# Optimization experiments

Measured on AMD Instinct MI355X. Metric: run time of the kernel, lower is better.

## Reference

```python
import jax, jax.numpy as jnp
import numpy as np

B, Q, K, H = 4, 512, 512, 256

def setup_inputs() -> dict:
    key = jax.random.key(0)
    ks = jax.random.split(key, 6)
    scale = 1.0 / np.sqrt(H)
    return {
        "queries": jax.random.normal(ks[0], (B, Q, H), dtype=jnp.float32),
        "keys": jax.random.normal(ks[1], (B, K, H), dtype=jnp.float32),
        "values": jax.random.normal(ks[2], (B, K, H), dtype=jnp.float32),
        "W_q": jax.random.normal(ks[3], (H, H), dtype=jnp.float32) * scale,
        "W_k": jax.random.normal(ks[4], (H, H), dtype=jnp.float32) * scale,
        "w_v": jax.random.normal(ks[5], (H,), dtype=jnp.float32) * scale,
    }

def reference(queries, keys, values, W_q, W_k, w_v):
    # Linear (no bias): x @ W.T, matching torch nn.Linear convention
    q = jnp.einsum('bqh,oh->bqo', queries, W_q)      # [B,Q,H]
    k = jnp.einsum('bkh,oh->bko', keys, W_k)          # [B,K,H]
    # broadcast add -> tanh -> linear reduce to scores [B,Q,K]
    features = jnp.tanh(q[:, :, None, :] + k[:, None, :, :])  # [B,Q,K,H]
    scores = jnp.einsum('bqkh,h->bqk', features, w_v)          # [B,Q,K]
    attn = jax.nn.softmax(scores, axis=-1)                     # [B,Q,K]
    # dropout p=0 (eval) -> identity
    return jnp.einsum('bqk,bkd->bqd', attn, values)            # [B,Q,Dv]
```

## Files before the change

### kernel.cpp

```cpp
#include <hip/hip_runtime.h>
#include <hip/hip_bf16.h>
#include <math.h>


#define B_ 4
#define Q_ 512
#define K_ 512
#define H_ 256
#define QE_ELEMS (B_ * Q_ * H_)
#define KE_ELEMS (B_ * H_ * K_)

static constexpr float CEXP = 2.8853900817779268f;
static constexpr float LOG2E = 1.4426950408889634f;

__device__ __forceinline__ float2 pk_fma(float2 a, float2 b, float2 c) {
    return make_float2(fmaf(a.x, b.x, c.x), fmaf(a.y, b.y, c.y));
}
__device__ __forceinline__ float2 pk_mul(float2 a, float2 b) {
    return make_float2(a.x * b.x, a.y * b.y);
}
__device__ __forceinline__ float2 bc2(float s) { return make_float2(s, s); }

#define PJ_AS(team, buf, dd, row) smem[(((team)*2 + (buf)) * 16 + (dd)) * 68 + (row)]
#define PJ_SS(team, buf, dd, row) smem[8704 + (((team)*2 + (buf)) * 16 + (dd)) * 68 + (row)]

__global__ __launch_bounds__(1024, 4) void proj_exp(
    const float* __restrict__ queries, const float* __restrict__ keys,
    const float* __restrict__ Wq, const float* __restrict__ Wk,
    float* __restrict__ qe, float* __restrict__ ke)
{
    __shared__ __align__(16) float smem[17408];

    const int bid = blockIdx.x;
    const int team = threadIdx.x >> 8;
    const int tid = threadIdx.x & 255;

    const float* A; const float* S; float* C; int ldc;
    if (bid < 128) {
        int mt = bid >> 2, nt = bid & 3;
        A = queries + (mt * 64) * H_;
        S = Wq + (nt * 64) * H_;
        C = qe + (mt * 64) * H_ + nt * 64;
        ldc = H_;
    } else {
        int id = bid - 128;
        int b = id >> 5, mt = (id >> 3) & 3, nt = id & 7;
        A = Wk + (mt * 64) * H_;
        S = keys + ((long)(b * K_ + nt * 64)) * H_;
        C = ke + ((long)(b * H_ + mt * 64)) * K_ + nt * 64;
        ldc = K_;
    }

    const int tx = tid & 15;
    const int ty = tid >> 4;
    const int ldr = tid >> 2;
    const int ldd = (tid & 3) * 4;
    const float* GA = A + ldr * H_ + team * 64 + ldd;
    const float* GS = S + ldr * H_ + team * 64 + ldd;

    float4 av = *(const float4*)GA;
    float4 sv = *(const float4*)GS;
    PJ_AS(team, 0, ldd + 0, ldr) = av.x; PJ_AS(team, 0, ldd + 1, ldr) = av.y;
    PJ_AS(team, 0, ldd + 2, ldr) = av.z; PJ_AS(team, 0, ldd + 3, ldr) = av.w;
    PJ_SS(team, 0, ldd + 0, ldr) = sv.x; PJ_SS(team, 0, ldd + 1, ldr) = sv.y;
    PJ_SS(team, 0, ldd + 2, ldr) = sv.z; PJ_SS(team, 0, ldd + 3, ldr) = sv.w;

    float acc[4][4] = {};
#pragma unroll
    for (int c = 0; c < 4; ++c) {
        const int cur = c & 1;
        if (c < 3) {
            av = *(const float4*)(GA + (c + 1) * 16);
            sv = *(const float4*)(GS + (c + 1) * 16);
        }
        __syncthreads();
#pragma unroll
        for (int dd = 0; dd < 16; ++dd) {
            float4 a4 = *(const float4*)&PJ_AS(team, cur, dd, ty * 4);
            float4 b4 = *(const float4*)&PJ_SS(team, cur, dd, tx * 4);
            float am[4] = {a4.x, a4.y, a4.z, a4.w};
            float bn[4] = {b4.x, b4.y, b4.z, b4.w};
#pragma unroll
            for (int i = 0; i < 4; ++i)
#pragma unroll
                for (int j = 0; j < 4; ++j)
                    acc[i][j] = fmaf(am[i], bn[j], acc[i][j]);
        }
        if (c < 3) {
            const int nxt = cur ^ 1;
            PJ_AS(team, nxt, ldd + 0, ldr) = av.x;
            PJ_AS(team, nxt, ldd + 1, ldr) = av.y;
            PJ_AS(team, nxt, ldd + 2, ldr) = av.z;
            PJ_AS(team, nxt, ldd + 3, ldr) = av.w;
            PJ_SS(team, nxt, ldd + 0, ldr) = sv.x;
            PJ_SS(team, nxt, ldd + 1, ldr) = sv.y;
            PJ_SS(team, nxt, ldd + 2, ldr) = sv.z;
            PJ_SS(team, nxt, ldd + 3, ldr) = sv.w;
        }
    }

    __syncthreads();
    if (team > 0) {
        float* Cmb = smem + (team - 1) * 4352;
#pragma unroll
        for (int i = 0; i < 4; ++i) {
            float4 o = {acc[i][0], acc[i][1], acc[i][2], acc[i][3]};
            *(float4*)&Cmb[(ty * 4 + i) * 68 + tx * 4] = o;
        }
    }
    __syncthreads();
    if (team == 0) {
#pragma unroll
        for (int i = 0; i < 4; ++i) {
            const int off = (ty * 4 + i) * 68 + tx * 4;
            float4 p1 = *(const float4*)&smem[off];
            float4 p2 = *(const float4*)&smem[4352 + off];
            float4 p3 = *(const float4*)&smem[8704 + off];
            float4 o;
            o.x = __builtin_amdgcn_exp2f(CEXP * (acc[i][0] + p1.x + p2.x + p3.x));
            o.y = __builtin_amdgcn_exp2f(CEXP * (acc[i][1] + p1.y + p2.y + p3.y));
            o.z = __builtin_amdgcn_exp2f(CEXP * (acc[i][2] + p1.z + p2.z + p3.z));
            o.w = __builtin_amdgcn_exp2f(CEXP * (acc[i][3] + p1.w + p2.w + p3.w));
            *(float4*)&C[(ty * 4 + i) * ldc + tx * 4] = o;
        }
    }
}

__global__ __launch_bounds__(1024, 8) void attn(
    const float* __restrict__ qe, const float* __restrict__ ke,
    const float* __restrict__ values, const float* __restrict__ wv,
    float* __restrict__ out)
{
    const int bid = blockIdx.x;
    const int xcd = bid & 7;
    const int b = xcd >> 1;
    const int q0 = (((bid >> 3) << 1) | (xcd & 1)) * 4;
    const int t = threadIdx.x;

    __shared__ __align__(16) float smem[9472];
    float* sQ  = smem;
    float* wvs = smem + 4 * H_;
    float* sS  = smem + 5 * H_;
    float* sP  = smem + 5 * H_ + 4 * K_;

    sQ[t] = qe[((long)(b * Q_ + q0 + (t >> 8))) * H_ + (t & 255)];
    if (t < H_) wvs[t] = wv[t];
    __syncthreads();

    {
        const int k2 = (t & 255) * 2;
        const int g = t >> 8;
        const float* keb = ke + ((long)(b * H_ + g * 64)) * K_ + k2;

        float2 nx0 = *(const float2*)(keb);
        float2 nx1 = *(const float2*)(keb + K_);
        float2 nx2 = *(const float2*)(keb + 2 * K_);
        float2 nx3 = *(const float2*)(keb + 3 * K_);
        float2 acc[4] = {};
        const float2 one2 = {1.0f, 1.0f};

#pragma unroll 2
        for (int hl = 0; hl < 64; hl += 4) {
            float2 c0 = nx0, c1 = nx1, c2 = nx2, c3 = nx3;
            if (hl < 60) {
                const float* p = keb + (hl + 4) * K_;
                nx0 = *(const float2*)(p);
                nx1 = *(const float2*)(p + K_);
                nx2 = *(const float2*)(p + 2 * K_);
                nx3 = *(const float2*)(p + 3 * K_);
            }
            const int h = g * 64 + hl;
            float4 w4 = *(const float4*)&wvs[h];
#pragma unroll
            for (int q = 0; q < 4; ++q) {
                float4 e = *(const float4*)&sQ[q * H_ + h];
                float2 t0 = pk_fma(bc2(e.x), c0, one2);
                float2 t1 = pk_fma(bc2(e.y), c1, one2);
                float2 t2 = pk_fma(bc2(e.z), c2, one2);
                float2 t3 = pk_fma(bc2(e.w), c3, one2);
                float2 d01 = pk_mul(t0, t1);
                float2 d23 = pk_mul(t2, t3);
                float2 n01 = pk_fma(bc2(w4.x), t1, pk_mul(bc2(w4.y), t0));
                float2 n23 = pk_fma(bc2(w4.z), t3, pk_mul(bc2(w4.w), t2));
                float2 num = pk_fma(n01, d23, pk_mul(n23, d01));
                float2 den = pk_mul(d01, d23);
                acc[q].x = fmaf(num.x, __builtin_amdgcn_rcpf(den.x), acc[q].x);
                acc[q].y = fmaf(num.y, __builtin_amdgcn_rcpf(den.y), acc[q].y);
            }
        }

        if (g > 0) {
            float* dst = sP + (g - 1) * 4 * K_;
#pragma unroll
            for (int q = 0; q < 4; ++q)
                *(float2*)&dst[q * K_ + k2] = acc[q];
        }
        __syncthreads();
        if (g == 0) {
#pragma unroll
            for (int q = 0; q < 4; ++q) {
                float2 p0 = *(const float2*)&sP[0 * 4 * K_ + q * K_ + k2];
                float2 p1 = *(const float2*)&sP[1 * 4 * K_ + q * K_ + k2];
                float2 p2 = *(const float2*)&sP[2 * 4 * K_ + q * K_ + k2];
                float2 o;
                o.x = -2.0f * (acc[q].x + p0.x + p1.x + p2.x);
                o.y = -2.0f * (acc[q].y + p0.y + p1.y + p2.y);
                *(float2*)&sS[q * K_ + k2] = o;
            }
        }
    }
    __syncthreads();

    if (t < 256) {
        const int lane = t & 63;
        const int q = t >> 6;
        float sv[8];
        float m = -INFINITY;
#pragma unroll
        for (int j = 0; j < 8; ++j) {
            sv[j] = sS[q * K_ + lane + 64 * j];
            m = fmaxf(m, sv[j]);
        }
#pragma unroll
        for (int off = 32; off >= 1; off >>= 1) m = fmaxf(m, __shfl_xor(m, off));
        float sum = 0.f;
#pragma unroll
        for (int j = 0; j < 8; ++j) {
            sv[j] = __builtin_amdgcn_exp2f((sv[j] - m) * LOG2E);
            sum += sv[j];
        }
#pragma unroll
        for (int off = 32; off >= 1; off >>= 1) sum += __shfl_xor(sum, off);
        float rs = 1.0f / sum;
#pragma unroll
        for (int j = 0; j < 8; ++j) sS[q * K_ + lane + 64 * j] = sv[j] * rs;
    }
    __syncthreads();

    {
        const int lane = t & 63;
        const int h4 = lane * 4;
        const int q = (t >> 6) & 3;
        const int kq = t >> 8;
        const float* vb = values + (long)b * K_ * H_ + h4;
        const float* sSq = sS + q * K_;
        float4 acc = {0.f, 0.f, 0.f, 0.f};
        const int kbeg = kq * 128;
#pragma unroll 2
        for (int k = kbeg; k < kbeg + 128; k += 4) {
            float4 a = *(const float4*)&sSq[k];
            float4 v0 = *(const float4*)&vb[(k + 0) * H_];
            float4 v1 = *(const float4*)&vb[(k + 1) * H_];
            float4 v2 = *(const float4*)&vb[(k + 2) * H_];
            float4 v3 = *(const float4*)&vb[(k + 3) * H_];
            acc.x = fmaf(a.x, v0.x, fmaf(a.y, v1.x, fmaf(a.z, v2.x, fmaf(a.w, v3.x, acc.x))));
            acc.y = fmaf(a.x, v0.y, fmaf(a.y, v1.y, fmaf(a.z, v2.y, fmaf(a.w, v3.y, acc.y))));
            acc.z = fmaf(a.x, v0.z, fmaf(a.y, v1.z, fmaf(a.z, v2.z, fmaf(a.w, v3.z, acc.z))));
            acc.w = fmaf(a.x, v0.w, fmaf(a.y, v1.w, fmaf(a.z, v2.w, fmaf(a.w, v3.w, acc.w))));
        }
        __syncthreads();
        float4* sRed = (float4*)sS;
        if (kq) sRed[(kq - 1) * 256 + q * 64 + lane] = acc;
        __syncthreads();
        if (kq == 0) {
            float4 p1 = sRed[q * 64 + lane];
            float4 p2 = sRed[256 + q * 64 + lane];
            float4 p3 = sRed[512 + q * 64 + lane];
            acc.x += p1.x + p2.x + p3.x;
            acc.y += p1.y + p2.y + p3.y;
            acc.z += p1.z + p2.z + p3.z;
            acc.w += p1.w + p2.w + p3.w;
            *(float4*)&out[((long)(b * Q_ + q0 + q)) * H_ + h4] = acc;
        }
    }
}

extern "C" void kernel_launch(void* const* d_in, const int* in_sizes, int n_in,
                              void* d_out, int out_size, void* d_ws, size_t ws_size,
                              hipStream_t stream) {
    const float* queries = (const float*)d_in[0];
    const float* keys    = (const float*)d_in[1];
    const float* values  = (const float*)d_in[2];
    const float* Wq      = (const float*)d_in[3];
    const float* Wk      = (const float*)d_in[4];
    const float* wv      = (const float*)d_in[5];
    float* out = (float*)d_out;

    float* qe = (float*)d_ws;
    float* ke = qe + QE_ELEMS;

    proj_exp<<<256, 1024, 0, stream>>>(queries, keys, Wq, Wk, qe, ke);
    attn<<<512, 1024, 0, stream>>>(qe, ke, values, wv, out);
}
```

Before: 129.7 us.

## Split attn-V product across 16 K-slices with all 4 queries per thread

The final attention-times-values stage now gives each wavefront a 32-key slice and all four query rows, so each loaded value row is reused four times instead of once. The first value loads are issued before the softmax barrier and later loads are software-pipelined one step ahead. Partial sums from the 16 slices are reduced through a larger shared-memory buffer. The cost is more shared memory per block (64KB instead of about 37KB), which may reduce occupancy, plus a heavier 16-way reduction.

```diff
diff --git a/kernel.cpp b/kernel.cpp
--- a/kernel.cpp
+++ b/kernel.cpp
@@ -137,7 +137,7 @@
     const int q0 = (((bid >> 3) << 1) | (xcd & 1)) * 4;
     const int t = threadIdx.x;
 
-    __shared__ __align__(16) float smem[9472];
+    __shared__ __align__(16) float smem[16384];
     float* sQ  = smem;
     float* wvs = smem + 4 * H_;
     float* sS  = smem + 5 * H_;
@@ -235,43 +235,57 @@
 #pragma unroll
         for (int j = 0; j < 8; ++j) sS[q * K_ + lane + 64 * j] = sv[j] * rs;
     }
+
+    const int lane3 = t & 63;
+    const int h4 = lane3 * 4;
+    const int kq = t >> 6;
+    const int kbeg = kq * 32;
+    const float* vb = values + (long)b * K_ * H_ + h4;
+
+    float4 nv0 = *(const float4*)&vb[(kbeg + 0) * H_];
+    float4 nv1 = *(const float4*)&vb[(kbeg + 1) * H_];
+    float4 nv2 = *(const float4*)&vb[(kbeg + 2) * H_];
+    float4 nv3 = *(const float4*)&vb[(kbeg + 3) * H_];
+
     __syncthreads();
 
     {
-        const int lane = t & 63;
-        const int h4 = lane * 4;
-        const int q = (t >> 6) & 3;
-        const int kq = t >> 8;
-        const float* vb = values + (long)b * K_ * H_ + h4;
-        const float* sSq = sS + q * K_;
-        float4 acc = {0.f, 0.f, 0.f, 0.f};
-        const int kbeg = kq * 128;
+        float4 acc[4] = {{0.f,0.f,0.f,0.f},{0.f,0.f,0.f,0.f},
+                         {0.f,0.f,0.f,0.f},{0.f,0.f,0.f,0.f}};
 #pragma unroll 2
-        for (int k = kbeg; k < kbeg + 128; k += 4) {
-            float4 a = *(const float4*)&sSq[k];
-            float4 v0 = *(const float4*)&vb[(k + 0) * H_];
-            float4 v1 = *(const float4*)&vb[(k + 1) * H_];
-            float4 v2 = *(const float4*)&vb[(k + 2) * H_];
-            float4 v3 = *(const float4*)&vb[(k + 3) * H_];
-            acc.x = fmaf(a.x, v0.x, fmaf(a.y, v1.x, fmaf(a.z, v2.x, fmaf(a.w, v3.x, acc.x))));
-            acc.y = fmaf(a.x, v0.y, fmaf(a.y, v1.y, fmaf(a.z, v2.y, fmaf(a.w, v3.y, acc.y))));
-            acc.z = fmaf(a.x, v0.z, fmaf(a.y, v1.z, fmaf(a.z, v2.z, fmaf(a.w, v3.z, acc.z))));
-            acc.w = fmaf(a.x, v0.w, fmaf(a.y, v1.w, fmaf(a.z, v2.w, fmaf(a.w, v3.w, acc.w))));
-        }
+        for (int k = kbeg; k < kbeg + 32; k += 4) {
+            float4 c0 = nv0, c1 = nv1, c2 = nv2, c3 = nv3;
+            if (k + 4 < kbeg + 32) {
+                const float* p = vb + (k + 4) * H_;
+                nv0 = *(const float4*)(p);
+                nv1 = *(const float4*)(p + H_);
+                nv2 = *(const float4*)(p + 2 * H_);
+                nv3 = *(const float4*)(p + 3 * H_);
+            }
+#pragma unroll
+            for (int q = 0; q < 4; ++q) {
+                float4 a = *(const float4*)&sS[q * K_ + k];
+                acc[q].x = fmaf(a.x, c0.x, fmaf(a.y, c1.x, fmaf(a.z, c2.x, fmaf(a.w, c3.x, acc[q].x))));
+                acc[q].y = fmaf(a.x, c0.y, fmaf(a.y, c1.y, fmaf(a.z, c2.y, fmaf(a.w, c3.y, acc[q].y))));
+                acc[q].z = fmaf(a.x, c0.z, fmaf(a.y, c1.z, fmaf(a.z, c2.z, fmaf(a.w, c3.z, acc[q].z))));
+                acc[q].w = fmaf(a.x, c0.w, fmaf(a.y, c1.w, fmaf(a.z, c2.w, fmaf(a.w, c3.w, acc[q].w))));
+            }
+        }
+
         __syncthreads();
-        float4* sRed = (float4*)sS;
-        if (kq) sRed[(kq - 1) * 256 + q * 64 + lane] = acc;
+        float* sRed = smem;
+#pragma unroll
+        for (int q = 0; q < 4; ++q)
+            *(float4*)&sRed[(kq * 4 + q) * 256 + h4] = acc[q];
         __syncthreads();
-        if (kq == 0) {
-            float4 p1 = sRed[q * 64 + lane];
-            float4 p2 = sRed[256 + q * 64 + lane];
-            float4 p3 = sRed[512 + q * 64 + lane];
-            acc.x += p1.x + p2.x + p3.x;
-            acc.y += p1.y + p2.y + p3.y;
-            acc.z += p1.z + p2.z + p3.z;
-            acc.w += p1.w + p2.w + p3.w;
-            *(float4*)&out[((long)(b * Q_ + q0 + q)) * H_ + h4] = acc;
-        }
+
+        const int q = t >> 8;
+        const int h = t & 255;
+        float s = 0.f;
+#pragma unroll
+        for (int kk = 0; kk < 16; ++kk)
+            s += sRed[(kk * 4 + q) * 256 + h];
+        out[((long)(b * Q_ + q0 + q)) * H_ + h] = s;
     }
 }
 
```

Measured after the change: 226.6 us. 1.75x slower.
